# Kernel tuning notes

Measured on AMD Instinct MI355X. Metric: run time of the kernel, lower is better.

The kernel has to match this reference:

```python
import jax, jax.numpy as jnp
import numpy as np

EMBED_DIM = 1024
NUM_HEADS = 16
HEAD_DIM = EMBED_DIM // NUM_HEADS
MAX_SEQ_LEN = 2048
B, T = 2, 2048


def setup_inputs() -> dict:
    key = jax.random.key(0)
    ks = jax.random.split(key, 12)
    d = EMBED_DIM
    s = lambda fan_in: 1.0 / np.sqrt(fan_in)
    return {
        "x": jax.random.normal(ks[0], (B, T, d), dtype=jnp.float32),
        "ln1_g": jnp.ones((d,), jnp.float32),
        "ln1_b": jnp.zeros((d,), jnp.float32),
        "w_attn": jax.random.normal(ks[1], (d, 3 * d), jnp.float32) * s(d),
        "b_attn": jnp.zeros((3 * d,), jnp.float32),
        "w_proj": jax.random.normal(ks[2], (d, d), jnp.float32) * s(d),
        "b_proj": jnp.zeros((d,), jnp.float32),
        "ln2_g": jnp.ones((d,), jnp.float32),
        "ln2_b": jnp.zeros((d,), jnp.float32),
        "w_fc": jax.random.normal(ks[3], (d, 4 * d), jnp.float32) * s(d),
        "b_fc": jnp.zeros((4 * d,), jnp.float32),
        "w_fc2": jax.random.normal(ks[4], (4 * d, d), jnp.float32) * s(4 * d),
        "b_fc2": jnp.zeros((d,), jnp.float32),
    }


def _layernorm(x, g, b, eps=1e-5):
    mu = jnp.mean(x, axis=-1, keepdims=True)
    var = jnp.var(x, axis=-1, keepdims=True)
    return (x - mu) * jax.lax.rsqrt(var + eps) * g + b


def _attention(x, w_attn, b_attn, w_proj, b_proj):
    b, t, c = x.shape
    qkv = x @ w_attn + b_attn  # [B,T,3C]
    q, k, v = jnp.split(qkv, 3, axis=-1)
    # [B,T,C] -> [B,H,T,Dh]
    rs = lambda a: a.reshape(b, t, NUM_HEADS, HEAD_DIM).transpose(0, 2, 1, 3)
    q, k, v = rs(q), rs(k), rs(v)
    wei = jnp.einsum("bhqd,bhkd->bhqk", q, k) * (HEAD_DIM ** -0.5)
    causal = jnp.tril(jnp.ones((t, t), bool))
    wei = jnp.where(causal, wei, -jnp.inf)
    wei = jax.nn.softmax(wei, axis=-1)  # attn_dropout is identity in eval mode
    out = jnp.einsum("bhqk,bhkd->bhqd", wei, v)
    out = out.transpose(0, 2, 1, 3).reshape(b, t, c)
    return out @ w_proj + b_proj  # resid_dropout identity in eval mode


def _ffn(x, w_fc, b_fc, w_fc2, b_fc2):
    h = jax.nn.gelu(x @ w_fc + b_fc, approximate=False)
    return h @ w_fc2 + b_fc2  # dropout identity in eval mode


def reference(x, ln1_g, ln1_b, w_attn, b_attn, w_proj, b_proj,
              ln2_g, ln2_b, w_fc, b_fc, w_fc2, b_fc2):
    x = x + _attention(_layernorm(x, ln1_g, ln1_b), w_attn, b_attn, w_proj, b_proj)
    x = x + _ffn(_layernorm(x, ln2_g, ln2_b), w_fc, b_fc, w_fc2, b_fc2)
    return x
```

## Files before the change

### kernel.cpp

```cpp
#include <hip/hip_runtime.h>

#define EMBED 1024
#define THREE_EMBED 3072
#define HEADS 16
#define HDIM 64
#define SEQ 2048
#define BATCH 2
#define MTOT 4096

typedef short bf16x8 __attribute__((ext_vector_type(8)));
typedef float f32x4 __attribute__((ext_vector_type(4)));

#define MFMA16(a, b, c) __builtin_amdgcn_mfma_f32_16x16x32_bf16(a, b, c, 0, 0, 0)

__device__ __forceinline__ unsigned short f2bf(float f) {
  union { float f; unsigned int u; } v; v.f = f;
  unsigned int r = v.u + 0x7fffu + ((v.u >> 16) & 1u);
  return (unsigned short)(r >> 16);
}

__device__ __forceinline__ void gload_lds16(const unsigned short* g, unsigned short* l) {
  __builtin_amdgcn_global_load_lds(
      (const __attribute__((address_space(1))) void*)g,
      (__attribute__((address_space(3))) void*)l, 16, 0, 0);
}

__device__ __forceinline__ void wait_vm0_barrier() {
  asm volatile("s_waitcnt vmcnt(0)" ::: "memory");
  __builtin_amdgcn_s_barrier();
}

template <int N>
__device__ __forceinline__ void wait_vmcnt() {
  if constexpr (N == 0) asm volatile("s_waitcnt vmcnt(0)" ::: "memory");
  else if constexpr (N == 1) asm volatile("s_waitcnt vmcnt(1)" ::: "memory");
  else if constexpr (N == 2) asm volatile("s_waitcnt vmcnt(2)" ::: "memory");
  else if constexpr (N == 3) asm volatile("s_waitcnt vmcnt(3)" ::: "memory");
  else if constexpr (N == 4) asm volatile("s_waitcnt vmcnt(4)" ::: "memory");
  else if constexpr (N == 6) asm volatile("s_waitcnt vmcnt(6)" ::: "memory");
  else if constexpr (N == 8) asm volatile("s_waitcnt vmcnt(8)" ::: "memory");
}

__global__ __launch_bounds__(256) void k_transpose_bf16(
    const float* __restrict__ in, unsigned short* __restrict__ out, int K, int N) {
  __shared__ float t[32][33];
  int tx = threadIdx.x & 31, ty = threadIdx.x >> 5;
  int n0 = blockIdx.x * 32, k0 = blockIdx.y * 32;
#pragma unroll
  for (int i = 0; i < 32; i += 8)
    t[ty + i][tx] = in[(size_t)(k0 + ty + i) * N + n0 + tx];
  __syncthreads();
#pragma unroll
  for (int i = 0; i < 32; i += 8)
    out[(size_t)(n0 + ty + i) * K + k0 + tx] = f2bf(t[tx][ty + i]);
}

__global__ __launch_bounds__(256) void k_transpose_v(
    const unsigned short* __restrict__ qkv, unsigned short* __restrict__ Vt) {
  __shared__ unsigned short t[32][33];
  int tx = threadIdx.x & 31, ty = threadIdx.x >> 5;
  int t0 = blockIdx.x * 32;
  int d0 = (blockIdx.y & 1) * 32;
  int bh = blockIdx.y >> 1;
  int b = bh >> 4, h = bh & 15;
  const unsigned short* src = qkv + (size_t)b * SEQ * THREE_EMBED + 2 * EMBED + h * HDIM;
#pragma unroll
  for (int i = 0; i < 32; i += 8)
    t[ty + i][tx] = src[(size_t)(t0 + ty + i) * THREE_EMBED + d0 + tx];
  __syncthreads();
  unsigned short* dst = Vt + (size_t)bh * HDIM * SEQ;
#pragma unroll
  for (int i = 0; i < 32; i += 8)
    dst[(size_t)(d0 + ty + i) * SEQ + t0 + tx] = t[tx][ty + i];
}

__global__ __launch_bounds__(256) void k_layernorm(
    const float* __restrict__ x, const float* __restrict__ g,
    const float* __restrict__ b, unsigned short* __restrict__ out) {
  int row = blockIdx.x;
  int tid = threadIdx.x;
  const float4 xv = *(const float4*)(x + (size_t)row * EMBED + tid * 4);
  float s = xv.x + xv.y + xv.z + xv.w;
  float sq = xv.x * xv.x + xv.y * xv.y + xv.z * xv.z + xv.w * xv.w;
#pragma unroll
  for (int off = 1; off < 64; off <<= 1) {
    s += __shfl_xor(s, off);
    sq += __shfl_xor(sq, off);
  }
  __shared__ float red[8];
  int w = tid >> 6;
  if ((tid & 63) == 0) { red[w] = s; red[4 + w] = sq; }
  __syncthreads();
  s = red[0] + red[1] + red[2] + red[3];
  sq = red[4] + red[5] + red[6] + red[7];
  float mu = s * (1.0f / EMBED);
  float var = sq * (1.0f / EMBED) - mu * mu;
  float rs = rsqrtf(var + 1e-5f);
  float xs[4] = {xv.x, xv.y, xv.z, xv.w};
  unsigned short o[4];
#pragma unroll
  for (int c = 0; c < 4; c++) {
    int col = tid * 4 + c;
    o[c] = f2bf((xs[c] - mu) * rs * g[col] + b[col]);
  }
  *(ushort4*)(out + (size_t)row * EMBED + tid * 4) = *(const ushort4*)o;
}

template <int EPI>
__global__ __launch_bounds__(512, 2) void k_gemm8(
    const unsigned short* __restrict__ A, const unsigned short* __restrict__ Bt,
    const float* __restrict__ bias, const float* __restrict__ resid,
    float* __restrict__ outf, unsigned short* __restrict__ outb,
    int M, int N, int K) {
  __shared__ unsigned short lA[2][16384];
  __shared__ unsigned short lB[2][16384];
  int tid = threadIdx.x;
  int nwg = gridDim.x * gridDim.y;
  int bid = blockIdx.y * gridDim.x + blockIdx.x;
  int swz = (bid & 7) * (nwg >> 3) + (bid >> 3);
  int m0 = (swz / gridDim.x) * 256, n0 = (swz % gridDim.x) * 256;
  int lane = tid & 63, w = tid >> 6;
  int lr = lane & 15, lg = lane >> 4;
  int warow = (w >> 2) * 64;
  int wbrow = (w & 3) * 32;
  int rx = lr & 7;
  int colk[2] = {(lg ^ rx) * 8, ((4 + lg) ^ rx) * 8};
  f32x4 acc[8][4] = {};
  int swzk = ((lane & 7) ^ ((lane >> 3) & 7)) * 8;
  const unsigned short* gA[2];
  const unsigned short* gB[2];
#pragma unroll
  for (int i = 0; i < 2; i++) {
    int chrow = (w * 2 + i) * 8 + (lane >> 3);
    gA[i] = A + (size_t)(m0 + chrow) * K + swzk;
    gB[i] = Bt + (size_t)(n0 + chrow) * K + swzk;
  }
  int NT = K >> 6;
  auto stage1 = [&](int sel, int kt, int nxt) {
    int h = sel >> 1;
    size_t goff = (size_t)(h * 128) * K + (size_t)kt * 64;
    int lo = h * 8192 + w * 1024;
    if ((sel & 1) == 0) {
      gload_lds16(gA[0] + goff, &lA[nxt][lo]);
      gload_lds16(gA[1] + goff, &lA[nxt][lo + 512]);
    } else {
      gload_lds16(gB[0] + goff, &lB[nxt][lo]);
      gload_lds16(gB[1] + goff, &lB[nxt][lo + 512]);
    }
  };
  bf16x8 afr[4][2], bfr[2][2];
  auto dsrd = [&](int cur, int mh, int nh) {
#pragma unroll
    for (int ii = 0; ii < 4; ii++) {
      int ra = mh * 128 + warow + ii * 16 + lr;
#pragma unroll
      for (int ks = 0; ks < 2; ks++)
        afr[ii][ks] = *(const bf16x8*)&lA[cur][ra * 64 + colk[ks]];
    }
#pragma unroll
    for (int jj = 0; jj < 2; jj++) {
      int rb = nh * 128 + wbrow + jj * 16 + lr;
#pragma unroll
      for (int ks = 0; ks < 2; ks++)
        bfr[jj][ks] = *(const bf16x8*)&lB[cur][rb * 64 + colk[ks]];
    }
  };
  auto domfma = [&](int mh, int nh) {
    __builtin_amdgcn_s_setprio(1);
#pragma unroll
    for (int ii = 0; ii < 4; ii++)
#pragma unroll
      for (int jj = 0; jj < 2; jj++)
#pragma unroll
        for (int ks = 0; ks < 2; ks++)
          acc[mh * 4 + ii][nh * 2 + jj] =
              MFMA16(afr[ii][ks], bfr[jj][ks], acc[mh * 4 + ii][nh * 2 + jj]);
    __builtin_amdgcn_s_setprio(0);
  };
  stage1(0, 0, 0); stage1(1, 0, 0); stage1(2, 0, 0); stage1(3, 0, 0);
  wait_vm0_barrier();
  for (int t = 0; t < NT - 1; t++) {
    int cur = t & 1, nxt = cur ^ 1;
    dsrd(cur, 0, 0); stage1(0, t + 1, nxt);
    asm volatile("s_waitcnt vmcnt(4)" ::: "memory");
    __builtin_amdgcn_s_barrier();
    domfma(0, 0);
    __builtin_amdgcn_s_barrier();
    dsrd(cur, 1, 0); stage1(1, t + 1, nxt);
    asm volatile("s_waitcnt vmcnt(4)" ::: "memory");
    __builtin_amdgcn_s_barrier();
    domfma(1, 0);
    __builtin_amdgcn_s_barrier();
    dsrd(cur, 0, 1); stage1(2, t + 1, nxt);
    __builtin_amdgcn_s_barrier();
    domfma(0, 1);
    __builtin_amdgcn_s_barrier();
    dsrd(cur, 1, 1); stage1(3, t + 1, nxt);
    asm volatile("s_waitcnt vmcnt(4)" ::: "memory");
    __builtin_amdgcn_s_barrier();
    domfma(1, 1);
    __builtin_amdgcn_s_barrier();
  }
  {
    int cur = (NT - 1) & 1;
    dsrd(cur, 0, 0);
    asm volatile("s_waitcnt vmcnt(2)" ::: "memory");
    __builtin_amdgcn_s_barrier();
    domfma(0, 0);
    __builtin_amdgcn_s_barrier();
    dsrd(cur, 1, 0);
    asm volatile("s_waitcnt vmcnt(0)" ::: "memory");
    __builtin_amdgcn_s_barrier();
    domfma(1, 0);
    __builtin_amdgcn_s_barrier();
    dsrd(cur, 0, 1); domfma(0, 1);
    dsrd(cur, 1, 1); domfma(1, 1);
  }
#pragma unroll
  for (int i = 0; i < 8; i++) {
#pragma unroll
    for (int j = 0; j < 4; j++) {
      int col = n0 + (j >> 1) * 128 + wbrow + (j & 1) * 16 + lr;
      float bv = bias[col];
#pragma unroll
      for (int r = 0; r < 4; r++) {
        int row = m0 + (i >> 2) * 128 + warow + (i & 3) * 16 + lg * 4 + r;
        float v = acc[i][j][r] + bv;
        size_t idx = (size_t)row * N + col;
        if constexpr (EPI == 0) {
          outb[idx] = f2bf(v);
        } else if constexpr (EPI == 1) {
          outf[idx] = v + resid[idx];
        } else {
          float gv = 0.5f * v * (1.0f + erff(v * 0.70710678118654752f));
          outb[idx] = f2bf(gv);
        }
      }
    }
  }
}

template <int EPI, int BN>
__global__ __launch_bounds__(256) void k_gemm(
    const unsigned short* __restrict__ A, const unsigned short* __restrict__ Bt,
    const float* __restrict__ bias, const float* __restrict__ resid,
    float* __restrict__ outf, unsigned short* __restrict__ outb,
    int M, int N, int K) {
  constexpr int BCH = BN / 16;
  constexpr int CHUNKS = 8 + BCH;
  constexpr int CPW = CHUNKS / 4;
  constexpr int MI = (BN == 128) ? 4 : 2;
  constexpr int NJ = 4;
  __shared__ unsigned short lA[3][128 * 32];
  __shared__ unsigned short lB[3][BN * 32];
  int tid = threadIdx.x;
  int nwg = gridDim.x * gridDim.y;
  int bid = blockIdx.y * gridDim.x + blockIdx.x;
  int swz = (bid & 7) * (nwg >> 3) + (bid >> 3);
  int m0 = (swz / gridDim.x) * 128, n0 = (swz % gridDim.x) * BN;
  int lane = tid & 63, w = tid >> 6;
  int wm = (BN == 128) ? (w >> 1) * 64 : w * 32;
  int wn = (BN == 128) ? (w & 1) * 64 : 0;
  int lr = lane & 15, lg = lane >> 4;
  f32x4 acc[MI][NJ] = {};
  int scol = ((lane & 3) ^ ((lane >> 3) & 3)) * 8;
  const unsigned short* gsrc[CPW];
  int loff[CPW];
  bool isa[CPW];
#pragma unroll
  for (int c0 = 0; c0 < CPW; c0++) {
    int c = w * CPW + c0;
    if (c < 8) {
      int row = c * 16 + (lane >> 2);
      gsrc[c0] = A + (size_t)(m0 + row) * K + scol;
      loff[c0] = c * 512;
      isa[c0] = true;
    } else {
      int row = (c - 8) * 16 + (lane >> 2);
      gsrc[c0] = Bt + (size_t)(n0 + row) * K + scol;
      loff[c0] = (c - 8) * 512;
      isa[c0] = false;
    }
  }
  auto stage = [&](int k0, int buf) {
#pragma unroll
    for (int c0 = 0; c0 < CPW; c0++)
      gload_lds16(gsrc[c0] + k0, isa[c0] ? &lA[buf][loff[c0]] : &lB[buf][loff[c0]]);
  };
  int fcol = (lg ^ ((lr >> 1) & 3)) * 8;
  auto compute = [&](int buf) {
    bf16x8 af[MI], bfr[NJ];
#pragma unroll
    for (int i = 0; i < MI; i++)
      af[i] = *(const bf16x8*)&lA[buf][(wm + i * 16 + lr) * 32 + fcol];
#pragma unroll
    for (int j = 0; j < NJ; j++)
      bfr[j] = *(const bf16x8*)&lB[buf][(wn + j * 16 + lr) * 32 + fcol];
    __builtin_amdgcn_s_setprio(1);
#pragma unroll
    for (int i = 0; i < MI; i++)
#pragma unroll
      for (int j = 0; j < NJ; j++)
        acc[i][j] = MFMA16(af[i], bfr[j], acc[i][j]);
    __builtin_amdgcn_s_setprio(0);
  };
  int nt = K >> 5;
  stage(0, 0);
  stage(32, 1);
  wait_vmcnt<CPW>();
  __builtin_amdgcn_s_barrier();
  int c0 = 0, c1 = 1, c2 = 2;
  for (int t = 0; t < nt - 2; t++) {
    stage((t + 2) * 32, c2);
    compute(c0);
    wait_vmcnt<CPW>();
    __builtin_amdgcn_s_barrier();
    int tmp = c0; c0 = c1; c1 = c2; c2 = tmp;
  }
  compute(c0);
  wait_vmcnt<0>();
  __builtin_amdgcn_s_barrier();
  compute(c1);
#pragma unroll
  for (int i = 0; i < MI; i++) {
#pragma unroll
    for (int j = 0; j < NJ; j++) {
      int colb = n0 + wn + j * 16 + lr;
      float bv = bias[colb];
#pragma unroll
      for (int r = 0; r < 4; r++) {
        int row = m0 + wm + i * 16 + lg * 4 + r;
        float v = acc[i][j][r] + bv;
        size_t idx = (size_t)row * N + colb;
        if constexpr (EPI == 0) {
          outb[idx] = f2bf(v);
        } else if constexpr (EPI == 1) {
          outf[idx] = v + resid[idx];
        } else {
          float gv = 0.5f * v * (1.0f + erff(v * 0.70710678118654752f));
          outb[idx] = f2bf(gv);
        }
      }
    }
  }
}

__global__ __launch_bounds__(256) void k_attention(
    const unsigned short* __restrict__ qkv, const unsigned short* __restrict__ Vt,
    unsigned short* __restrict__ out) {
  __shared__ unsigned short lK[2][64 * 64];
  __shared__ unsigned short lV[2][64 * 64];
  __shared__ unsigned short lP[4][16][72];
  int bid = blockIdx.x;
  int i = bid >> 3;
  int qt = 31 - (i >> 2);
  int bh = (bid & 7) * 4 + (i & 3);
  int b = bh >> 4, h = bh & 15;
  int tid = threadIdx.x, lane = tid & 63, w = tid >> 6;
  int lr = lane & 15, lg = lane >> 4;
  const unsigned short* base = qkv + (size_t)b * SEQ * THREE_EMBED + h * HDIM;
  const unsigned short* Kb = base + EMBED;
  const unsigned short* Vb = Vt + (size_t)bh * HDIM * SEQ;
  int q0 = qt * 64 + w * 16;
  bf16x8 qf[2];
  {
    int qrow = q0 + lr;
    qf[0] = *(const bf16x8*)(base + (size_t)qrow * THREE_EMBED + lg * 8);
    qf[1] = *(const bf16x8*)(base + (size_t)qrow * THREE_EMBED + 32 + lg * 8);
  }
  bf16x8 ones;
  {
    short o1 = 0x3F80;
#pragma unroll
    for (int j = 0; j < 8; j++) ones[j] = o1;
  }
  f32x4 o[4] = {};
  f32x4 osum = {};
  float m_[4] = {-INFINITY, -INFINITY, -INFINITY, -INFINITY};
  int srow = lane >> 3;
  int scol = ((lane & 7) ^ (lane >> 3)) * 8;
  const float SCL = 0.125f * 1.4426950408889634f;
  int nkv = qt + 1;
  auto stage = [&](int kt, int cur) {
#pragma unroll
    for (int c = 0; c < 2; c++) {
      int chunk = w * 2 + c;
      int row = chunk * 8 + srow;
      gload_lds16(Kb + (size_t)(kt * 64 + row) * THREE_EMBED + scol, &lK[cur][chunk * 512]);
      gload_lds16(Vb + (size_t)row * SEQ + kt * 64 + scol, &lV[cur][chunk * 512]);
    }
  };
  stage(0, 0);
  wait_vm0_barrier();
  int cur = 0;
  for (int kt = 0; kt < nkv; kt++) {
    if (kt + 1 < nkv) stage(kt + 1, cur ^ 1);
    __builtin_amdgcn_s_setprio(1);
    f32x4 s[4];
#pragma unroll
    for (int ct = 0; ct < 4; ct++) {
      int krow = ct * 16 + lr;
      int sw = (krow & 7) << 3;
      bf16x8 k0 = *(const bf16x8*)&lK[cur][krow * 64 + ((lg * 8) ^ sw)];
      bf16x8 k1 = *(const bf16x8*)&lK[cur][krow * 64 + ((32 + lg * 8) ^ sw)];
      f32x4 z = {};
      z = MFMA16(qf[0], k0, z);
      s[ct] = MFMA16(qf[1], k1, z);
    }
    __builtin_amdgcn_s_setprio(0);
    bool maskt = (kt * 64 + 63 > q0);
    float pm[4] = {-INFINITY, -INFINITY, -INFINITY, -INFINITY};
#pragma unroll
    for (int ct = 0; ct < 4; ct++) {
#pragma unroll
      for (int r = 0; r < 4; r++) {
        float sv = s[ct][r] * SCL;
        if (maskt) {
          int kg = kt * 64 + ct * 16 + lr;
          int qg = q0 + lg * 4 + r;
          if (kg > qg) sv = -INFINITY;
        }
        s[ct][r] = sv;
        pm[r] = fmaxf(pm[r], sv);
      }
    }
    float dm = fmaxf(fmaxf(pm[0] - m_[0], pm[1] - m_[1]),
                     fmaxf(pm[2] - m_[2], pm[3] - m_[3]));
    if (!__all(dm <= 8.0f)) {
#pragma unroll
      for (int r = 0; r < 4; r++) {
        float mx = pm[r];
        mx = fmaxf(mx, __shfl_xor(mx, 1));
        mx = fmaxf(mx, __shfl_xor(mx, 2));
        mx = fmaxf(mx, __shfl_xor(mx, 4));
        mx = fmaxf(mx, __shfl_xor(mx, 8));
        float mn = fmaxf(m_[r], mx);
        float al = exp2f(m_[r] - mn);
        m_[r] = mn;
        osum[r] *= al;
#pragma unroll
        for (int dt = 0; dt < 4; dt++) o[dt][r] *= al;
      }
    }
#pragma unroll
    for (int ct = 0; ct < 4; ct++)
#pragma unroll
      for (int r = 0; r < 4; r++)
        lP[w][lg * 4 + r][ct * 16 + lr] = f2bf(exp2f(s[ct][r] - m_[r]));
    __builtin_amdgcn_s_setprio(1);
#pragma unroll
    for (int ks = 0; ks < 2; ks++) {
      bf16x8 pf = *(const bf16x8*)&lP[w][lr][ks * 32 + lg * 8];
      osum = MFMA16(pf, ones, osum);
#pragma unroll
      for (int dt = 0; dt < 4; dt++) {
        int vrow = dt * 16 + lr;
        int sw = (vrow & 7) << 3;
        bf16x8 vf = *(const bf16x8*)&lV[cur][vrow * 64 + ((ks * 32 + lg * 8) ^ sw)];
        o[dt] = MFMA16(pf, vf, o[dt]);
      }
    }
    __builtin_amdgcn_s_setprio(0);
    wait_vm0_barrier();
    cur ^= 1;
  }
#pragma unroll
  for (int dt = 0; dt < 4; dt++)
#pragma unroll
    for (int r = 0; r < 4; r++) {
      int row = q0 + lg * 4 + r;
      float val = o[dt][r] / osum[r];
      out[(size_t)(b * SEQ + row) * EMBED + h * HDIM + dt * 16 + lr] = f2bf(val);
    }
}

extern "C" void kernel_launch(void* const* d_in, const int* in_sizes, int n_in,
                              void* d_out, int out_size, void* d_ws, size_t ws_size,
                              hipStream_t stream) {
  const float* x      = (const float*)d_in[0];
  const float* ln1_g  = (const float*)d_in[1];
  const float* ln1_b  = (const float*)d_in[2];
  const float* w_attn = (const float*)d_in[3];
  const float* b_attn = (const float*)d_in[4];
  const float* w_proj = (const float*)d_in[5];
  const float* b_proj = (const float*)d_in[6];
  const float* ln2_g  = (const float*)d_in[7];
  const float* ln2_b  = (const float*)d_in[8];
  const float* w_fc   = (const float*)d_in[9];
  const float* b_fc   = (const float*)d_in[10];
  const float* w_fc2  = (const float*)d_in[11];
  const float* b_fc2  = (const float*)d_in[12];
  float* outp = (float*)d_out;

  char* ws = (char*)d_ws;
  unsigned short* wT_attn = (unsigned short*)(ws);
  unsigned short* wT_proj = (unsigned short*)(ws + 6291456);
  unsigned short* wT_fc   = (unsigned short*)(ws + 8388608);
  unsigned short* wT_fc2  = (unsigned short*)(ws + 16777216);
  unsigned short* buf1    = (unsigned short*)(ws + 25165824);
  float*          x1      = (float*)(ws + 33554432);
  unsigned short* Vt      = (unsigned short*)(ws + 33554432);
  unsigned short* qkv_h   = (unsigned short*)(ws + 50331648);

  dim3 blk(256);
  k_transpose_bf16<<<dim3(3072 / 32, 1024 / 32), blk, 0, stream>>>(w_attn, wT_attn, 1024, 3072);
  k_transpose_bf16<<<dim3(1024 / 32, 1024 / 32), blk, 0, stream>>>(w_proj, wT_proj, 1024, 1024);
  k_transpose_bf16<<<dim3(4096 / 32, 1024 / 32), blk, 0, stream>>>(w_fc, wT_fc, 1024, 4096);
  k_transpose_bf16<<<dim3(1024 / 32, 4096 / 32), blk, 0, stream>>>(w_fc2, wT_fc2, 4096, 1024);
  k_layernorm<<<dim3(MTOT), blk, 0, stream>>>(x, ln1_g, ln1_b, buf1);
  k_gemm8<0><<<dim3(THREE_EMBED / 256, MTOT / 256), dim3(512), 0, stream>>>(
      buf1, wT_attn, b_attn, nullptr, nullptr, qkv_h, MTOT, THREE_EMBED, EMBED);
  k_transpose_v<<<dim3(SEQ / 32, 2 * BATCH * HEADS), blk, 0, stream>>>(qkv_h, Vt);
  k_attention<<<dim3(1024), blk, 0, stream>>>(qkv_h, Vt, buf1);
  k_gemm<1, 64><<<dim3(EMBED / 64, MTOT / 128), blk, 0, stream>>>(
      buf1, wT_proj, b_proj, x, x1, nullptr, MTOT, EMBED, EMBED);
  k_layernorm<<<dim3(MTOT), blk, 0, stream>>>(x1, ln2_g, ln2_b, buf1);
  k_gemm8<2><<<dim3(4 * EMBED / 256, MTOT / 256), dim3(512), 0, stream>>>(
      buf1, wT_fc, b_fc, nullptr, nullptr, qkv_h, MTOT, 4 * EMBED, EMBED);
  k_gemm<1, 64><<<dim3(EMBED / 64, MTOT / 128), blk, 0, stream>>>(
      qkv_h, wT_fc2, b_fc2, x1, outp, nullptr, MTOT, EMBED, 4 * EMBED);
}
```

Before: 270.3 us.

## Restructure GEMM main loop into register-reusing four-phase schedule with fewer barriers

Rewrites the 256x256 bf16 GEMM inner loop so A and B fragments are held in separate register sets (aX/aY, b0/b1) and reused across quadrants. The old schedule reloaded both operands for every quadrant, and the new one uses a snake order (00,01,11,10) that loads each half once per k-tile. Global-to-LDS staging is interleaved per quadrant with one barrier per phase instead of two. The next tile's A fragment is prefetched from the other buffer before the last MFMA phase. This should cut LDS read traffic and barrier stalls, at the cost of more VGPRs and a subtler ordering of LDS hazards.

```diff
diff --git a/kernel.cpp b/kernel.cpp
--- a/kernel.cpp
+++ b/kernel.cpp
@@ -39,6 +39,11 @@
   else if constexpr (N == 4) asm volatile("s_waitcnt vmcnt(4)" ::: "memory");
   else if constexpr (N == 6) asm volatile("s_waitcnt vmcnt(6)" ::: "memory");
   else if constexpr (N == 8) asm volatile("s_waitcnt vmcnt(8)" ::: "memory");
+}
+
+__device__ __forceinline__ void open_phase_barrier() {
+  __builtin_amdgcn_s_barrier();
+  __builtin_amdgcn_sched_barrier(0);
 }
 
 __global__ __launch_bounds__(256) void k_transpose_bf16(
@@ -136,36 +141,38 @@
     gB[i] = Bt + (size_t)(n0 + chrow) * K + swzk;
   }
   int NT = K >> 6;
-  auto stage1 = [&](int sel, int kt, int nxt) {
-    int h = sel >> 1;
+  auto stageA = [&](int h, int kt, int buf) {
     size_t goff = (size_t)(h * 128) * K + (size_t)kt * 64;
     int lo = h * 8192 + w * 1024;
-    if ((sel & 1) == 0) {
-      gload_lds16(gA[0] + goff, &lA[nxt][lo]);
-      gload_lds16(gA[1] + goff, &lA[nxt][lo + 512]);
-    } else {
-      gload_lds16(gB[0] + goff, &lB[nxt][lo]);
-      gload_lds16(gB[1] + goff, &lB[nxt][lo + 512]);
-    }
-  };
-  bf16x8 afr[4][2], bfr[2][2];
-  auto dsrd = [&](int cur, int mh, int nh) {
+    gload_lds16(gA[0] + goff, &lA[buf][lo]);
+    gload_lds16(gA[1] + goff, &lA[buf][lo + 512]);
+  };
+  auto stageB = [&](int h, int kt, int buf) {
+    size_t goff = (size_t)(h * 128) * K + (size_t)kt * 64;
+    int lo = h * 8192 + w * 1024;
+    gload_lds16(gB[0] + goff, &lB[buf][lo]);
+    gload_lds16(gB[1] + goff, &lB[buf][lo + 512]);
+  };
+  bf16x8 aX[4][2], aY[4][2], b0[2][2], b1[2][2];
+  auto rdA = [&](int buf, int mh, bf16x8 (&dst)[4][2]) {
 #pragma unroll
     for (int ii = 0; ii < 4; ii++) {
       int ra = mh * 128 + warow + ii * 16 + lr;
 #pragma unroll
       for (int ks = 0; ks < 2; ks++)
-        afr[ii][ks] = *(const bf16x8*)&lA[cur][ra * 64 + colk[ks]];
-    }
+        dst[ii][ks] = *(const bf16x8*)&lA[buf][ra * 64 + colk[ks]];
+    }
+  };
+  auto rdB = [&](int buf, int nh, bf16x8 (&dst)[2][2]) {
 #pragma unroll
     for (int jj = 0; jj < 2; jj++) {
       int rb = nh * 128 + wbrow + jj * 16 + lr;
 #pragma unroll
       for (int ks = 0; ks < 2; ks++)
-        bfr[jj][ks] = *(const bf16x8*)&lB[cur][rb * 64 + colk[ks]];
-    }
-  };
-  auto domfma = [&](int mh, int nh) {
+        dst[jj][ks] = *(const bf16x8*)&lB[buf][rb * 64 + colk[ks]];
+    }
+  };
+  auto mf = [&](int mh, int nh, bf16x8 (&aa)[4][2], bf16x8 (&bb)[2][2]) {
     __builtin_amdgcn_s_setprio(1);
 #pragma unroll
     for (int ii = 0; ii < 4; ii++)
@@ -174,47 +181,49 @@
 #pragma unroll
         for (int ks = 0; ks < 2; ks++)
           acc[mh * 4 + ii][nh * 2 + jj] =
-              MFMA16(afr[ii][ks], bfr[jj][ks], acc[mh * 4 + ii][nh * 2 + jj]);
+              MFMA16(aa[ii][ks], bb[jj][ks], acc[mh * 4 + ii][nh * 2 + jj]);
     __builtin_amdgcn_s_setprio(0);
   };
-  stage1(0, 0, 0); stage1(1, 0, 0); stage1(2, 0, 0); stage1(3, 0, 0);
-  wait_vm0_barrier();
+  stageA(0, 0, 0); stageB(0, 0, 0); stageB(1, 0, 0); stageA(1, 0, 0);
+  wait_vmcnt<6>();
+  open_phase_barrier();
+  rdA(0, 0, aX);
   for (int t = 0; t < NT - 1; t++) {
     int cur = t & 1, nxt = cur ^ 1;
-    dsrd(cur, 0, 0); stage1(0, t + 1, nxt);
-    asm volatile("s_waitcnt vmcnt(4)" ::: "memory");
-    __builtin_amdgcn_s_barrier();
-    domfma(0, 0);
-    __builtin_amdgcn_s_barrier();
-    dsrd(cur, 1, 0); stage1(1, t + 1, nxt);
-    asm volatile("s_waitcnt vmcnt(4)" ::: "memory");
-    __builtin_amdgcn_s_barrier();
-    domfma(1, 0);
-    __builtin_amdgcn_s_barrier();
-    dsrd(cur, 0, 1); stage1(2, t + 1, nxt);
-    __builtin_amdgcn_s_barrier();
-    domfma(0, 1);
-    __builtin_amdgcn_s_barrier();
-    dsrd(cur, 1, 1); stage1(3, t + 1, nxt);
-    asm volatile("s_waitcnt vmcnt(4)" ::: "memory");
-    __builtin_amdgcn_s_barrier();
-    domfma(1, 1);
-    __builtin_amdgcn_s_barrier();
+    stageA(0, t + 1, nxt);
+    wait_vmcnt<4>();
+    open_phase_barrier();
+    rdB(cur, 0, b0);
+    rdB(cur, 1, b1);
+    mf(0, 0, aX, b0);
+    stageB(0, t + 1, nxt);
+    wait_vmcnt<4>();
+    open_phase_barrier();
+    rdA(cur, 1, aY);
+    mf(0, 1, aX, b1);
+    stageB(1, t + 1, nxt);
+    wait_vmcnt<4>();
+    open_phase_barrier();
+    mf(1, 1, aY, b1);
+    stageA(1, t + 1, nxt);
+    wait_vmcnt<4>();
+    open_phase_barrier();
+    rdA(nxt, 0, aX);
+    mf(1, 0, aY, b0);
   }
   {
     int cur = (NT - 1) & 1;
-    dsrd(cur, 0, 0);
-    asm volatile("s_waitcnt vmcnt(2)" ::: "memory");
-    __builtin_amdgcn_s_barrier();
-    domfma(0, 0);
-    __builtin_amdgcn_s_barrier();
-    dsrd(cur, 1, 0);
-    asm volatile("s_waitcnt vmcnt(0)" ::: "memory");
-    __builtin_amdgcn_s_barrier();
-    domfma(1, 0);
-    __builtin_amdgcn_s_barrier();
-    dsrd(cur, 0, 1); domfma(0, 1);
-    dsrd(cur, 1, 1); domfma(1, 1);
+    wait_vmcnt<2>();
+    open_phase_barrier();
+    rdB(cur, 0, b0);
+    rdB(cur, 1, b1);
+    mf(0, 0, aX, b0);
+    wait_vmcnt<0>();
+    open_phase_barrier();
+    rdA(cur, 1, aY);
+    mf(0, 1, aX, b1);
+    mf(1, 1, aY, b1);
+    mf(1, 0, aY, b0);
   }
 #pragma unroll
   for (int i = 0; i < 8; i++) {
```

Measured after the change: 256.2 us. -5.2%, faster.
